# Performance work log

Measured on AMD Instinct MI355X. Metric: run time of the kernel, lower is better.

The kernel has to match this reference:

```python
import jax, jax.numpy as jnp
import numpy as np

NUM_HEADS = 16
HEAD_DIM = 64
HIDDEN = 1024
ROPE_BASE = 10000.0


def _rope_cache(seq_len, dtype):
    inv_freq = 1.0 / (ROPE_BASE ** (jnp.arange(0, HEAD_DIM, 2, dtype=jnp.float32) / HEAD_DIM))
    freqs = jnp.arange(seq_len, dtype=jnp.float32)[:, None] * inv_freq[None, :]  # [S, D/2]
    emb = jnp.concatenate([freqs, freqs], axis=-1)  # [S, D]
    return jnp.cos(emb).astype(dtype), jnp.sin(emb).astype(dtype)


def _rotate_half(x):
    x1, x2 = jnp.split(x, 2, axis=-1)
    return jnp.concatenate([-x2, x1], axis=-1)


def setup_inputs() -> dict:
    key = jax.random.key(0)
    k1, k2, k3 = jax.random.split(key, 3)
    B, S = 1, 4096
    x = jax.random.normal(k1, (B, S, HIDDEN), dtype=jnp.float32)
    w_qkv = jax.random.normal(k2, (3 * HIDDEN, HIDDEN), dtype=jnp.float32) * (1.0 / np.sqrt(HIDDEN))
    w_out = jax.random.normal(k3, (HIDDEN, HIDDEN), dtype=jnp.float32) * (1.0 / np.sqrt(HIDDEN))
    return {"x": x, "w_qkv": w_qkv, "w_out": w_out}


def reference(x, w_qkv, w_out):
    B, S, _ = x.shape
    scale = 1.0 / np.sqrt(HEAD_DIM)
    # fused QKV projection (torch Linear: x @ W^T)
    qkv = jnp.einsum('bsd,ed->bse', x, w_qkv)
    qkv = qkv.reshape(B, S, 3, NUM_HEADS, HEAD_DIM).transpose(2, 0, 3, 1, 4)
    q, k, v = qkv[0], qkv[1], qkv[2]  # [B, H, S, Dh]
    cos, sin = _rope_cache(S, x.dtype)  # [S, Dh]
    cos = cos[None, None]
    sin = sin[None, None]
    q = q * cos + _rotate_half(q) * sin
    k = k * cos + _rotate_half(k) * sin
    scores = jnp.einsum('bhqd,bhkd->bhqk', q, k) * scale  # [B, H, S, S]
    causal = jnp.triu(jnp.ones((S, S), dtype=bool), k=1)
    min_val = jnp.finfo(scores.dtype).min
    scores = jnp.where(causal[None, None], min_val, scores)
    attn = jax.nn.softmax(scores, axis=-1)
    out = jnp.einsum('bhqk,bhkd->bhqd', attn, v)  # [B, H, S, Dh]
    out = out.transpose(0, 2, 1, 3).reshape(B, S, HIDDEN)
    return jnp.einsum('bsd,ed->bse', out, w_out)
```

## Files before the change

kernel.cpp:

```cpp
#include <hip/hip_runtime.h>

#define S_LEN 4096
#define NHEAD 16
#define DHEAD 64
#define HID 1024

typedef float f32x4 __attribute__((ext_vector_type(4)));
typedef float f32x16 __attribute__((ext_vector_type(16)));
typedef unsigned short u16x8 __attribute__((ext_vector_type(8)));
typedef __bf16 bf16x8 __attribute__((ext_vector_type(8)));

__device__ __forceinline__ unsigned short f2bf(float f) {
  union { float f; unsigned u; } x; x.f = f;
  return (unsigned short)((x.u + 0x7FFFu + ((x.u >> 16) & 1u)) >> 16);
}
__device__ __forceinline__ float bf2f(unsigned short u) {
  union { unsigned u; float f; } x; x.u = ((unsigned)u) << 16;
  return x.f;
}
__device__ __forceinline__ f32x4 mfma16(u16x8 a, u16x8 b, f32x4 c) {
  return __builtin_amdgcn_mfma_f32_16x16x32_bf16(
      __builtin_bit_cast(bf16x8, a), __builtin_bit_cast(bf16x8, b), c, 0, 0, 0);
}
__device__ __forceinline__ f32x16 mfma32(u16x8 a, u16x8 b, f32x16 c) {
  return __builtin_amdgcn_mfma_f32_32x32x16_bf16(
      __builtin_bit_cast(bf16x8, a), __builtin_bit_cast(bf16x8, b), c, 0, 0, 0);
}
__device__ __forceinline__ void gload16(const void* g, void* l) {
  __builtin_amdgcn_global_load_lds(
      (const __attribute__((address_space(1))) void*)g,
      (__attribute__((address_space(3))) void*)l, 16, 0, 0);
}
__device__ __forceinline__ void permswap(unsigned& a, unsigned& b) {
#if __has_builtin(__builtin_amdgcn_permlane32_swap)
  typedef unsigned u32x2 __attribute__((ext_vector_type(2)));
  u32x2 r = __builtin_amdgcn_permlane32_swap(a, b, false, false);
  a = r[0]; b = r[1];
#else
  asm volatile("v_permlane32_swap_b32 %0, %1" : "+v"(a), "+v"(b));
#endif
}
__device__ __forceinline__ unsigned cvtpk(float lo, float hi) {
  unsigned r;
  asm("v_cvt_pk_bf16_f32 %0, %1, %2" : "=v"(r) : "v"(lo), "v"(hi));
  return r;
}
__device__ __forceinline__ float fexp2(float x) {
  float r;
  asm("v_exp_f32 %0, %1" : "=v"(r) : "v"(x));
  return r;
}

__global__ void k_cvt_all(const float4* __restrict__ x, const float4* __restrict__ wq,
                          const float4* __restrict__ wo, ushort4* __restrict__ xb,
                          ushort4* __restrict__ wqb, ushort4* __restrict__ wob) {
  int i = blockIdx.x * blockDim.x + threadIdx.x;
  const float4* src; ushort4* dst; int off;
  if (i < 1048576)      { src = x;  dst = xb;  off = i; }
  else if (i < 1835008) { src = wq; dst = wqb; off = i - 1048576; }
  else                  { src = wo; dst = wob; off = i - 1835008; }
  float4 v = src[off];
  ushort4 o;
  o.x = f2bf(v.x); o.y = f2bf(v.y); o.z = f2bf(v.z); o.w = f2bf(v.w);
  dst[off] = o;
}

__global__ void k_rope_split(const unsigned short* __restrict__ qkv,
                             unsigned short* __restrict__ Q,
                             unsigned short* __restrict__ Kf) {
  int s = blockIdx.x;
  int t = threadIdx.x;
  int h = t >> 5, i = t & 31;
  float inv = fexp2(-(float)i * 0.4152410118609203f);
  float ang = (float)s * inv;
  float sn, cs;
  __sincosf(ang, &sn, &cs);
  const unsigned short* row = qkv + (size_t)s * 3072;
  float q1 = bf2f(row[h * 64 + i]);
  float q2 = bf2f(row[h * 64 + i + 32]);
  float k1 = bf2f(row[1024 + h * 64 + i]);
  float k2 = bf2f(row[1024 + h * 64 + i + 32]);
  const float ksc = 0.125f * 1.44269504f;
  size_t qo = ((size_t)h * S_LEN + s) * 64 + i;
  Q[qo]      = f2bf(q1 * cs - q2 * sn);
  Q[qo + 32] = f2bf(q2 * cs + q1 * sn);
  int t32 = s >> 5, kv = s & 31;
  size_t ko = ((((size_t)h * 128 + t32) * 4 + (i >> 4)) * 2 + ((i >> 3) & 1)) * 256 + kv * 8 + (i & 7);
  Kf[ko]        = f2bf((k1 * cs - k2 * sn) * ksc);
  Kf[ko + 1024] = f2bf((k2 * cs + k1 * sn) * ksc);
}

__global__ void k_vt(const unsigned short* __restrict__ qkv,
                     unsigned short* __restrict__ Vf) {
  __shared__ unsigned short tile[64][65];
  int st = blockIdx.x, h = blockIdx.y;
  int t = threadIdx.x;
  int r = t >> 2, c0 = (t & 3) * 16;
  const unsigned short* src = qkv + (size_t)(st * 64 + r) * 3072 + 2048 + h * 64 + c0;
  u16x8 a = *(const u16x8*)src;
  u16x8 b = *(const u16x8*)(src + 8);
#pragma unroll
  for (int j = 0; j < 8; ++j) { tile[r][c0 + j] = a[j]; tile[r][c0 + 8 + j] = b[j]; }
  __syncthreads();
#pragma unroll
  for (int pass = 0; pass < 2; ++pass) {
    int task = t + pass * 256;
    int o = task >> 6, d = task & 63;
    int t32 = st * 2 + (o >> 2), kc = (o >> 1) & 1, hfv = o & 1;
    u16x8 v;
#pragma unroll
    for (int e = 0; e < 8; ++e) v[e] = tile[o * 8 + e][d];
    *(u16x8*)(Vf + (((((size_t)h * 128 + t32) * 2 + kc) * 2 + hfv) * 64 + d) * 8) = v;
  }
}

__device__ __forceinline__ void stc(float* p, float v) { *p = v; }
__device__ __forceinline__ void stc(unsigned short* p, float v) { *p = f2bf(v); }

template <typename OutT>
__global__ __launch_bounds__(256, 5) void gemm_bt(
    const unsigned short* __restrict__ A, const unsigned short* __restrict__ B,
    OutT* __restrict__ C, int M, int N, int K) {
  __shared__ __attribute__((aligned(16))) unsigned short As[2][128][32];
  __shared__ __attribute__((aligned(16))) unsigned short Bs[2][128][32];
  const int tid = threadIdx.x;
  const int w = tid >> 6, lane = tid & 63;
  const int bm = blockIdx.y * 128, bn = blockIdx.x * 128;
  const int wr = w >> 1, wc = w & 1;
  const int l16 = lane >> 2;
  const int c4 = (lane & 3) * 8;
  f32x4 acc[4][4] = {};

  auto stage = [&](int buf, int k0) {
#pragma unroll
    for (int c = 0; c < 2; ++c) {
      int row = w * 32 + c * 16;
      gload16(A + (size_t)(bm + row + l16) * K + k0 + c4, &As[buf][row][0]);
      gload16(B + (size_t)(bn + row + l16) * K + k0 + c4, &Bs[buf][row][0]);
    }
  };

  const int nk = K >> 5;
  stage(0, 0);
  int cur = 0;
  for (int kt = 0; kt < nk; ++kt) {
    __syncthreads();
    if (kt + 1 < nk) stage(cur ^ 1, (kt + 1) << 5);
    u16x8 af[4], bfr[4];
#pragma unroll
    for (int m = 0; m < 4; ++m)
      af[m] = *(const u16x8*)&As[cur][wr * 64 + m * 16 + (lane & 15)][(lane >> 4) * 8];
#pragma unroll
    for (int n = 0; n < 4; ++n)
      bfr[n] = *(const u16x8*)&Bs[cur][wc * 64 + n * 16 + (lane & 15)][(lane >> 4) * 8];
#pragma unroll
    for (int m = 0; m < 4; ++m)
#pragma unroll
      for (int n = 0; n < 4; ++n)
        acc[m][n] = mfma16(af[m], bfr[n], acc[m][n]);
    cur ^= 1;
  }
#pragma unroll
  for (int m = 0; m < 4; ++m) {
    int row = bm + wr * 64 + m * 16 + (lane >> 4) * 4;
#pragma unroll
    for (int n = 0; n < 4; ++n) {
      int col = bn + wc * 64 + n * 16 + (lane & 15);
#pragma unroll
      for (int j = 0; j < 4; ++j) stc(&C[(size_t)(row + j) * N + col], acc[m][n][j]);
    }
  }
}

__device__ __forceinline__ void attn_range(
    const unsigned short* __restrict__ kfb, const unsigned short* __restrict__ vfb,
    const u16x8* qf, f32x16& accA, f32x16& accB, float& l_own,
    int t0, int t1, int nst, int qg, int hf, int kOffBase, int vOffBase) {
  u16x8 ka[4], kb_[4], kc2[4], va[4], vb_[4], vc2[4];
#define LOADK(dst, t)                                                         \
  {                                                                           \
    const unsigned short* p_ = kfb + (size_t)(t) * 2048 + kOffBase;           \
    dst[0] = *(const u16x8*)(p_);                                             \
    dst[1] = *(const u16x8*)(p_ + 512);                                       \
    dst[2] = *(const u16x8*)(p_ + 1024);                                      \
    dst[3] = *(const u16x8*)(p_ + 1536);                                      \
  }
#define LOADV(dst, t)                                                         \
  {                                                                           \
    const unsigned short* p_ = vfb + (size_t)(t) * 2048 + vOffBase;           \
    dst[0] = *(const u16x8*)(p_);                                             \
    dst[1] = *(const u16x8*)(p_ + 256);                                       \
    dst[2] = *(const u16x8*)(p_ + 1024);                                      \
    dst[3] = *(const u16x8*)(p_ + 1280);                                      \
  }
#define STEP(t, kc_, vc_, kn_, vn_)                                           \
  {                                                                           \
    const int tn = ((t) + 2 < t1) ? (t) + 2 : t1 - 1;                         \
    LOADK(kn_, tn);                                                           \
    LOADV(vn_, tn);                                                           \
    f32x16 sc = {};                                                           \
    __builtin_amdgcn_s_setprio(1);                                            \
    _Pragma("unroll") for (int c = 0; c < 4; ++c) sc = mfma32(kc_[c], qf[c], sc); \
    __builtin_amdgcn_s_setprio(0);                                            \
    if ((t) == nst - 1) {                     \
      _Pragma("unroll") for (int r = 0; r < 16; ++r) {                        \
        int kvl = (t) * 32 + (r & 3) + 8 * (r >> 2) + 4 * hf;                 \
        if (kvl > qg) sc[r] = -1e30f;                                         \
      }                                                                       \
    }                                                                         \
    float p[16];                                                              \
    _Pragma("unroll") for (int r = 0; r < 16; ++r) p[r] = fexp2(sc[r]);       \
    l_own += (((p[0] + p[1]) + (p[2] + p[3])) + ((p[4] + p[5]) + (p[6] + p[7]))) + \
             (((p[8] + p[9]) + (p[10] + p[11])) + ((p[12] + p[13]) + (p[14] + p[15]))); \
    unsigned dw[8];                                                           \
    _Pragma("unroll") for (int k = 0; k < 8; ++k) dw[k] = cvtpk(p[2 * k], p[2 * k + 1]); \
    __builtin_amdgcn_s_setprio(1);                                            \
    _Pragma("unroll") for (int kc = 0; kc < 2; ++kc) {                        \
      unsigned x0 = dw[4 * kc + 0], x1 = dw[4 * kc + 1];                      \
      unsigned y0 = dw[4 * kc + 2], y1 = dw[4 * kc + 3];                      \
      permswap(x0, y0);                                                       \
      permswap(x1, y1);                                                       \
      union { u16x8 v; unsigned u[4]; } pf;                                   \
      pf.u[0] = x0; pf.u[1] = x1; pf.u[2] = y0; pf.u[3] = y1;                 \
      accA = mfma32(vc_[kc * 2 + 0], pf.v, accA);                             \
      accB = mfma32(vc_[kc * 2 + 1], pf.v, accB);                             \
    }                                                                         \
    __builtin_amdgcn_s_setprio(0);                                            \
  }

  LOADK(ka, t0);
  LOADV(va, t0);
  {
    const int t1c = (t0 + 1 < t1) ? t0 + 1 : t1 - 1;
    LOADK(kb_, t1c);
    LOADV(vb_, t1c);
  }
  int t = t0;
  while (true) {
    STEP(t, ka, va, kc2, vc2);
    if (++t >= t1) break;
    STEP(t, kb_, vb_, ka, va);
    if (++t >= t1) break;
    STEP(t, kc2, vc2, kb_, vb_);
    if (++t >= t1) break;
  }
#undef STEP
#undef LOADK
#undef LOADV
}

__device__ __forceinline__ void attn_epilogue(
    const f32x16& accA, const f32x16& accB, float l_own, char* eb,
    unsigned short* __restrict__ O, int h, int qb, int wr, int q31, int hf) {
  float l_run;
  {
    unsigned a = __float_as_uint(l_own), b = a;
    permswap(a, b);
    l_run = __uint_as_float(a) + __uint_as_float(b);
  }
  const float inv = 1.0f / l_run;
#pragma unroll
  for (int dblk = 0; dblk < 2; ++dblk) {
#pragma unroll
    for (int tt = 0; tt < 4; ++tt) {
      float a0, a1, a2, a3;
      if (dblk == 0) { a0 = accA[4 * tt]; a1 = accA[4 * tt + 1]; a2 = accA[4 * tt + 2]; a3 = accA[4 * tt + 3]; }
      else           { a0 = accB[4 * tt]; a1 = accB[4 * tt + 1]; a2 = accB[4 * tt + 2]; a3 = accB[4 * tt + 3]; }
      unsigned d0 = cvtpk(a0 * inv, a1 * inv);
      unsigned d1 = cvtpk(a2 * inv, a3 * inv);
      int dbase = dblk * 32 + 8 * tt + 4 * hf;
      int off = (q31 * 128 + dbase * 2) ^ ((q31 & 7) << 4);
      *(uint2*)(eb + off) = make_uint2(d0, d1);
    }
  }
  const int lane = hf * 32 + q31;
#pragma unroll
  for (int pass = 0; pass < 4; ++pass) {
    int q = (lane >> 3) + pass * 8;
    int c8 = lane & 7;
    u16x8 vv = *(const u16x8*)(eb + ((q * 128 + c8 * 16) ^ ((q & 7) << 4)));
    *(u16x8*)(O + (size_t)(qb + wr * 32 + q) * HID + h * 64 + c8 * 8) = vv;
  }
}

__global__ __launch_bounds__(512) void flash_attn(
    const unsigned short* __restrict__ Q,
    const unsigned short* __restrict__ Kf,
    const unsigned short* __restrict__ Vf,
    unsigned short* __restrict__ O) {
  __shared__ __attribute__((aligned(16))) unsigned short ebuf[8][2048];
  __shared__ float part[4][64][33];
  const int tid = threadIdx.x;
  const int wv = tid >> 6, lane = tid & 63;
  const int wr = wv & 3, role = wv >> 2;
  const int q31 = lane & 31, hf = lane >> 5;
  const int h = blockIdx.x;
  const int p = blockIdx.y;
  const int tileB = 31 - p;
  const int nstA = 4 * p + wr + 1;
  const int nstB = 4 * tileB + wr + 1;
  const int cut = 62 - 4 * p;

  const unsigned short* kfb = Kf + (size_t)h * 128 * 2048;
  const unsigned short* vfb = Vf + (size_t)h * 128 * 2048;
  const int kOffBase = hf * 256 + q31 * 8;
  const int vOffBase = hf * 512 + q31 * 8;
  char* eb = (char*)&ebuf[wv][0];

  const int qgB = tileB * 128 + wr * 32 + q31;
  u16x8 qfB[4];
  {
    const unsigned short* qp = Q + ((size_t)h * S_LEN + qgB) * 64 + hf * 8;
#pragma unroll
    for (int c = 0; c < 4; ++c) qfB[c] = *(const u16x8*)(qp + c * 16);
  }

  if (role == 0) {
    const int qgA = p * 128 + wr * 32 + q31;
    u16x8 qfA[4];
    {
      const unsigned short* qp = Q + ((size_t)h * S_LEN + qgA) * 64 + hf * 8;
#pragma unroll
      for (int c = 0; c < 4; ++c) qfA[c] = *(const u16x8*)(qp + c * 16);
    }
    f32x16 accA = {}, accB = {};
    float l_own = 0.f;
    attn_range(kfb, vfb, qfA, accA, accB, l_own, 0, nstA, nstA, qgA, hf, kOffBase, vOffBase);
    attn_epilogue(accA, accB, l_own, eb, O, h, p * 128, wr, q31, hf);
    f32x16 bA = {}, bB = {};
    float bl = 0.f;
    attn_range(kfb, vfb, qfB, bA, bB, bl, 0, cut, nstB, qgB, hf, kOffBase, vOffBase);
    float* pp = &part[wr][lane][0];
#pragma unroll
    for (int r = 0; r < 16; ++r) { pp[r] = bA[r]; pp[16 + r] = bB[r]; }
    pp[32] = bl;
    __syncthreads();
  } else {
    f32x16 bA = {}, bB = {};
    float bl = 0.f;
    attn_range(kfb, vfb, qfB, bA, bB, bl, cut, nstB, nstB, qgB, hf, kOffBase, vOffBase);
    __syncthreads();
    const float* pp = &part[wr][lane][0];
#pragma unroll
    for (int r = 0; r < 16; ++r) { bA[r] += pp[r]; bB[r] += pp[16 + r]; }
    bl += pp[32];
    attn_epilogue(bA, bB, bl, eb, O, h, tileB * 128, wr, q31, hf);
  }
}

extern "C" void kernel_launch(void* const* d_in, const int* in_sizes, int n_in,
                              void* d_out, int out_size, void* d_ws, size_t ws_size,
                              hipStream_t stream) {
  const float* x = (const float*)d_in[0];
  const float* w_qkv = (const float*)d_in[1];
  const float* w_out = (const float*)d_in[2];
  float* out = (float*)d_out;
  char* ws = (char*)d_ws;

  unsigned short* xb    = (unsigned short*)(ws + 0);
  unsigned short* wqkvb = (unsigned short*)(ws + 8388608);
  unsigned short* woutb = (unsigned short*)(ws + 14680064);
  unsigned short* qkvb  = (unsigned short*)(ws + 16777216);
  unsigned short* Qb    = (unsigned short*)(ws + 41943040);
  unsigned short* Kfb   = (unsigned short*)(ws + 50331648);
  unsigned short* Vfb   = (unsigned short*)(ws + 58720256);
  unsigned short* attnb = (unsigned short*)(ws + 67108864);

  k_cvt_all<<<dim3(8192), dim3(256), 0, stream>>>(
      (const float4*)x, (const float4*)w_qkv, (const float4*)w_out,
      (ushort4*)xb, (ushort4*)wqkvb, (ushort4*)woutb);

  gemm_bt<unsigned short><<<dim3(24, 32), dim3(256), 0, stream>>>(xb, wqkvb, qkvb, 4096, 3072, 1024);

  k_rope_split<<<dim3(4096), dim3(512), 0, stream>>>(qkvb, Qb, Kfb);
  k_vt<<<dim3(64, 16), dim3(256), 0, stream>>>(qkvb, Vfb);

  flash_attn<<<dim3(16, 16), dim3(512), 0, stream>>>(Qb, Kfb, Vfb, attnb);

  gemm_bt<float><<<dim3(8, 32), dim3(256), 0, stream>>>(attnb, woutb, out, 4096, 1024, 1024);
}
```

Before: 156.3 us.

## Triple-buffer GEMM LDS staging with vmcnt waits and XOR-swizzled layout

```diff
diff --git a/kernel.cpp b/kernel.cpp
--- a/kernel.cpp
+++ b/kernel.cpp
@@ -118,47 +118,61 @@
 __device__ __forceinline__ void stc(unsigned short* p, float v) { *p = f2bf(v); }
 
 template <typename OutT>
-__global__ __launch_bounds__(256, 5) void gemm_bt(
+__global__ __launch_bounds__(256, 3) void gemm_bt(
     const unsigned short* __restrict__ A, const unsigned short* __restrict__ B,
     OutT* __restrict__ C, int M, int N, int K) {
-  __shared__ __attribute__((aligned(16))) unsigned short As[2][128][32];
-  __shared__ __attribute__((aligned(16))) unsigned short Bs[2][128][32];
+  __shared__ __attribute__((aligned(16))) unsigned short As[3][128][32];
+  __shared__ __attribute__((aligned(16))) unsigned short Bs[3][128][32];
   const int tid = threadIdx.x;
   const int w = tid >> 6, lane = tid & 63;
   const int bm = blockIdx.y * 128, bn = blockIdx.x * 128;
   const int wr = w >> 1, wc = w & 1;
   const int l16 = lane >> 2;
-  const int c4 = (lane & 3) * 8;
+  const int c4s = ((lane & 3) ^ ((lane >> 3) & 3)) * 8;
   f32x4 acc[4][4] = {};
 
-  auto stage = [&](int buf, int k0) {
+  auto stage = [&](int buf, int kt) {
+    const int k0 = kt << 5;
 #pragma unroll
     for (int c = 0; c < 2; ++c) {
       int row = w * 32 + c * 16;
-      gload16(A + (size_t)(bm + row + l16) * K + k0 + c4, &As[buf][row][0]);
-      gload16(B + (size_t)(bn + row + l16) * K + k0 + c4, &Bs[buf][row][0]);
+      gload16(A + (size_t)(bm + row + l16) * K + k0 + c4s, &As[buf][row][0]);
+      gload16(B + (size_t)(bn + row + l16) * K + k0 + c4s, &Bs[buf][row][0]);
     }
   };
 
   const int nk = K >> 5;
   stage(0, 0);
+  stage(1, 1);
   int cur = 0;
   for (int kt = 0; kt < nk; ++kt) {
-    __syncthreads();
-    if (kt + 1 < nk) stage(cur ^ 1, (kt + 1) << 5);
+    asm volatile("s_waitcnt vmcnt(4)" ::: "memory");
+    __builtin_amdgcn_sched_barrier(0);
+    __builtin_amdgcn_s_barrier();
+    __builtin_amdgcn_sched_barrier(0);
+    {
+      const int sbuf = (cur + 2 >= 3) ? cur - 1 : cur + 2;
+      const int stile = (kt + 2 < nk) ? kt + 2 : nk - 1;
+      stage(sbuf, stile);
+    }
+    const int sph = (((lane >> 4) ^ (lane >> 1)) & 3) * 16;
     u16x8 af[4], bfr[4];
 #pragma unroll
-    for (int m = 0; m < 4; ++m)
-      af[m] = *(const u16x8*)&As[cur][wr * 64 + m * 16 + (lane & 15)][(lane >> 4) * 8];
-#pragma unroll
-    for (int n = 0; n < 4; ++n)
-      bfr[n] = *(const u16x8*)&Bs[cur][wc * 64 + n * 16 + (lane & 15)][(lane >> 4) * 8];
+    for (int m = 0; m < 4; ++m) {
+      int row = wr * 64 + m * 16 + (lane & 15);
+      af[m] = *(const u16x8*)((const char*)&As[cur][0][0] + row * 64 + sph);
+    }
+#pragma unroll
+    for (int n = 0; n < 4; ++n) {
+      int row = wc * 64 + n * 16 + (lane & 15);
+      bfr[n] = *(const u16x8*)((const char*)&Bs[cur][0][0] + row * 64 + sph);
+    }
 #pragma unroll
     for (int m = 0; m < 4; ++m)
 #pragma unroll
       for (int n = 0; n < 4; ++n)
         acc[m][n] = mfma16(af[m], bfr[n], acc[m][n]);
-    cur ^= 1;
+    cur = (cur + 1 == 3) ? 0 : cur + 1;
   }
 #pragma unroll
   for (int m = 0; m < 4; ++m) {
```

Result: faster. 130.1 us (-16.8%).
